# Kernel optimization log

Hardware: AMD Instinct MI355X
Metric: run time of the kernel (lower is better)

The kernel has to match this reference:

```python
import jax, jax.numpy as jnp
import numpy as np

B, TAPE, N, F = 128, 100000, 50000, 32

def setup_inputs() -> dict:
    key = jax.random.key(0)
    k1, k2, k3, k4 = jax.random.split(key, 4)
    tape = jax.random.normal(k1, (B, TAPE), dtype=jnp.float32)
    input_indices = jax.random.randint(k2, (N, F), 0, TAPE)
    # He init scaled by fan-in, padding slots (index==0) zeroed as in __init__
    weights = jax.random.normal(k3, (N, F), dtype=jnp.float32) * jnp.sqrt(2.0 / F)
    weights = jnp.where(input_indices == 0, 0.0, weights)
    bias = jnp.zeros((N,), dtype=jnp.float32)
    output_indices = jnp.arange(N)
    act_type = jax.random.randint(k4, (N,), 0, 2)
    return {"tape": tape, "weights": weights, "bias": bias,
            "input_indices": input_indices, "output_indices": output_indices,
            "act_type": act_type}

def reference(tape, weights, bias, input_indices, output_indices, act_type):
    # gather padded fan-in inputs: [B, N, F]
    gathered = tape[:, input_indices]
    # weighted sum over fan-in + bias: [B, N]
    x = jnp.einsum('bnf,nf->bn', gathered, weights) + bias
    # per-activation-type apply (two activation groups: relu / tanh)
    x = jnp.where(act_type == 0, jax.nn.relu(x), jnp.tanh(x))
    # scatter results back into tape
    return tape.at[:, output_indices].set(x)
```

## Files before the change

### kernel.cpp

```cpp
#include <hip/hip_runtime.h>
#include <cmath>

#define TAPE_SZ 100000
#define N_SZ    50000
#define F_SZ    32
#define B_SZ    128
#define GSUB    64
#define RANGE   25000
#define NBV     128
#define NCHUNK  391
#define GRID_G  (NCHUNK*2)

static __device__ __forceinline__ unsigned short f32_to_bf16(float f) {
    unsigned int u = __float_as_uint(f);
    u = (u + 0x7fffu + ((u >> 16) & 1u)) >> 16;
    return (unsigned short)u;
}

__global__ __launch_bounds__(256) void transpose_g64(const float* __restrict__ in,
                                                     unsigned short* __restrict__ outG,
                                                     float* __restrict__ out) {
    __shared__ float tile[32][129];
    const int x0 = blockIdx.x * 32;
    const int tx = threadIdx.x;
    const int ty = threadIdx.y;

    #pragma unroll
    for (int yy = ty; yy < B_SZ; yy += 8)
        tile[tx][yy] = in[(size_t)yy * TAPE_SZ + x0 + tx];
    __syncthreads();

    const int tid = ty * 32 + tx;
    const int l = tid >> 3;
    const int o = tid & 7;
    const int g = o >> 2;
    const int j = o & 3;
    unsigned short* dst = outG + ((size_t)g * TAPE_SZ + x0 + l) * GSUB + j * 16;
    union { unsigned short u[8]; uint4 q; } p0, p1;
    #pragma unroll
    for (int k = 0; k < 8; ++k) {
        p0.u[k] = f32_to_bf16(tile[l][g * GSUB + j * 16 + k]);
        p1.u[k] = f32_to_bf16(tile[l][g * GSUB + j * 16 + 8 + k]);
    }
    *(uint4*)dst       = p0.q;
    *(uint4*)(dst + 8) = p1.q;

    if (x0 + tx >= N_SZ) {
        #pragma unroll
        for (int yy = ty; yy < B_SZ; yy += 8)
            out[(size_t)yy * TAPE_SZ + x0 + tx] = tile[tx][yy];
    }
}

__global__ __launch_bounds__(512, 4) void gather_g64(
    const unsigned short* __restrict__ tapeG,
    const float* __restrict__ weights,
    const float* __restrict__ bias,
    const int*   __restrict__ in_idx,
    const int*   __restrict__ out_idx,
    const int*   __restrict__ act_type,
    float* __restrict__ out) {
    __shared__ union {
        struct {
            uint2 ent[NBV][33];
            int   start[NBV][5];
        } s;
        float x[GSUB][132];
    } u;
    __shared__ int   s_oidx[NBV];
    __shared__ float s_bias[NBV];
    __shared__ int   s_act[NBV];

    const int tid   = threadIdx.x;
    const int g     = blockIdx.x & 1;
    const int chunk = blockIdx.x >> 1;
    const int n0    = chunk * NBV;
    const int nend  = min(NBV, N_SZ - n0);

    if (tid < NBV) {
        if (tid < nend) {
            const int*   ip = in_idx  + (size_t)(n0 + tid) * 32;
            const float* wp = weights + (size_t)(n0 + tid) * 32;
            int ix[32];
            #pragma unroll
            for (int f = 0; f < 32; ++f) ix[f] = ip[f];
            int c0 = 0, c1 = 0, c2 = 0, c3 = 0;
            #pragma unroll
            for (int f = 0; f < 32; ++f) {
                const int r = ix[f] / RANGE;
                c0 += (r == 0); c1 += (r == 1); c2 += (r == 2); c3 += (r == 3);
            }
            int o0 = 0, o1 = c0, o2 = c0 + c1, o3 = c0 + c1 + c2;
            u.s.start[tid][0] = 0;  u.s.start[tid][1] = o1;
            u.s.start[tid][2] = o2; u.s.start[tid][3] = o3;
            u.s.start[tid][4] = 32;
            #pragma unroll
            for (int f = 0; f < 32; ++f) {
                const int r = ix[f] / RANGE;
                int pos;
                if      (r == 0) pos = o0++;
                else if (r == 1) pos = o1++;
                else if (r == 2) pos = o2++;
                else             pos = o3++;
                u.s.ent[tid][pos] = make_uint2((unsigned)ix[f], __float_as_uint(wp[f]));
            }
            s_oidx[tid] = out_idx[n0 + tid];
            s_bias[tid] = bias[n0 + tid];
            s_act[tid]  = act_type[n0 + tid];
        } else {
            #pragma unroll
            for (int r = 0; r < 5; ++r) u.s.start[tid][r] = 0;
        }
    }
    __syncthreads();

    const int nl = tid >> 2;
    const int q  = tid & 3;
    const unsigned short* tg = tapeG + (size_t)g * TAPE_SZ * GSUB + q * 16;

    float a[16];
    #pragma unroll
    for (int k = 0; k < 16; ++k) a[k] = 0.f;

    #pragma unroll 1
    for (int r = 0; r < 4; ++r) {
        const int e1 = u.s.start[nl][r + 1];
        for (int e = u.s.start[nl][r]; e < e1; ++e) {
            const uint2 iw = u.s.ent[nl][e];
            const unsigned short* p = tg + (size_t)iw.x * GSUB;
            const uint4 q0 = *(const uint4*)(p);
            const uint4 q1 = *(const uint4*)(p + 8);
            const float wv = __uint_as_float(iw.y);
#define ACC8(Q, B0) \
            a[B0+0] = fmaf(__uint_as_float((Q).x << 16),          wv, a[B0+0]); \
            a[B0+1] = fmaf(__uint_as_float((Q).x & 0xffff0000u),  wv, a[B0+1]); \
            a[B0+2] = fmaf(__uint_as_float((Q).y << 16),          wv, a[B0+2]); \
            a[B0+3] = fmaf(__uint_as_float((Q).y & 0xffff0000u),  wv, a[B0+3]); \
            a[B0+4] = fmaf(__uint_as_float((Q).z << 16),          wv, a[B0+4]); \
            a[B0+5] = fmaf(__uint_as_float((Q).z & 0xffff0000u),  wv, a[B0+5]); \
            a[B0+6] = fmaf(__uint_as_float((Q).w << 16),          wv, a[B0+6]); \
            a[B0+7] = fmaf(__uint_as_float((Q).w & 0xffff0000u),  wv, a[B0+7]);
            ACC8(q0, 0) ACC8(q1, 8)
#undef ACC8
        }
        __syncthreads();
    }

    {
        const float bz = (nl < nend) ? s_bias[nl] : 0.f;
        const int   at = (nl < nend) ? s_act[nl]  : 0;
        #pragma unroll
        for (int k = 0; k < 16; ++k) {
            const float v = a[k] + bz;
            a[k] = (at == 0) ? fmaxf(v, 0.f) : tanhf(v);
        }
    }
    __syncthreads();
    if (nl < nend) {
        #pragma unroll
        for (int k = 0; k < 16; ++k)
            u.x[q * 16 + k][nl] = a[k];
    }
    __syncthreads();

    const int quads = (nend + 3) >> 2;
    for (int it = tid; it < GSUB * quads; it += 512) {
        int bsub, j4;
        if (nend == NBV) { bsub = it >> 5; j4 = it & 31; }
        else             { bsub = it / quads; j4 = it - bsub * quads; }
        const int nq  = j4 * 4;
        const int oc0 = s_oidx[nq];
        float* orow = out + (size_t)(g * GSUB + bsub) * TAPE_SZ;
        const bool consec = (nq + 3 < nend) &&
                            (s_oidx[nq + 1] == oc0 + 1) &&
                            (s_oidx[nq + 2] == oc0 + 2) &&
                            (s_oidx[nq + 3] == oc0 + 3) && ((oc0 & 3) == 0);
        if (consec) {
            *(float4*)(orow + oc0) = *(const float4*)&u.x[bsub][nq];
        } else {
            #pragma unroll
            for (int c = 0; c < 4; ++c)
                if (nq + c < nend) orow[s_oidx[nq + c]] = u.x[bsub][nq + c];
        }
    }
}

__global__ __launch_bounds__(128) void gather_fallback(const float* __restrict__ tape,
                                                       const float* __restrict__ weights,
                                                       const float* __restrict__ bias,
                                                       const int*   __restrict__ in_idx,
                                                       const int*   __restrict__ out_idx,
                                                       const int*   __restrict__ act_type,
                                                       float* __restrict__ out) {
    const int n = blockIdx.x;
    const int b = threadIdx.x;
    float acc = 0.f;
    for (int f = 0; f < F_SZ; ++f) {
        acc += tape[(size_t)b * TAPE_SZ + in_idx[(size_t)n * F_SZ + f]] *
               weights[(size_t)n * F_SZ + f];
    }
    acc += bias[n];
    acc = (act_type[n] == 0) ? fmaxf(acc, 0.f) : tanhf(acc);
    out[(size_t)b * TAPE_SZ + out_idx[n]] = acc;
}

__global__ __launch_bounds__(256) void copy_tail_fb(const float* __restrict__ tape,
                                                    float* __restrict__ out) {
    const int n4 = (TAPE_SZ - N_SZ) / 4;
    int i = blockIdx.x * blockDim.x + threadIdx.x;
    int b = blockIdx.y;
    if (i < n4) {
        const float4* src = (const float4*)(tape + (size_t)b * TAPE_SZ + N_SZ);
        float4*       dst = (float4*)(out  + (size_t)b * TAPE_SZ + N_SZ);
        dst[i] = src[i];
    }
}

extern "C" void kernel_launch(void* const* d_in, const int* in_sizes, int n_in,
                              void* d_out, int out_size, void* d_ws, size_t ws_size,
                              hipStream_t stream) {
    const float* tape    = (const float*)d_in[0];
    const float* weights = (const float*)d_in[1];
    const float* bias    = (const float*)d_in[2];
    const int*   in_idx  = (const int*)d_in[3];
    const int*   out_idx = (const int*)d_in[4];
    const int*   act     = (const int*)d_in[5];
    float*       out     = (float*)d_out;

    const size_t need = (size_t)TAPE_SZ * B_SZ * sizeof(unsigned short);
    if (ws_size >= need) {
        unsigned short* tapeG = (unsigned short*)d_ws;
        transpose_g64<<<dim3(TAPE_SZ / 32), dim3(32, 8), 0, stream>>>(tape, tapeG, out);
        gather_g64<<<dim3(GRID_G), dim3(512), 0, stream>>>(
            tapeG, weights, bias, in_idx, out_idx, act, out);
    } else {
        copy_tail_fb<<<dim3(((TAPE_SZ - N_SZ) / 4 + 255) / 256, B_SZ), 256, 0, stream>>>(tape, out);
        gather_fallback<<<dim3(N_SZ), 128, 0, stream>>>(
            tape, weights, bias, in_idx, out_idx, act, out);
    }
}
```

Before: 197.3 us.

## Store full 128-batch bf16 rows per tape entry and gather once per neuron

The transposed bf16 tape changes from two 64-batch halves to one contiguous 256-byte row per tape index. The gather kernel now processes all 128 batches per block, so each neuron's index list is sorted and read once instead of twice. Bucketing widens from 4 to 8 tape ranges using packed byte counters, giving finer locality phases separated by block barriers. Each thread handles two neurons with paired loads for more memory-level parallelism, and the occupancy hint rises to 8 blocks per CU, which risks register pressure and more barrier overhead.

Result: faster. 185.5 us (-6.0%).

```diff
diff --git a/kernel.cpp b/kernel.cpp
--- a/kernel.cpp
+++ b/kernel.cpp
@@ -5,11 +5,10 @@
 #define N_SZ    50000
 #define F_SZ    32
 #define B_SZ    128
-#define GSUB    64
-#define RANGE   25000
-#define NBV     128
-#define NCHUNK  391
-#define GRID_G  (NCHUNK*2)
+#define NRANGE  8
+#define RANGE   12500
+#define NBV     64
+#define NCHUNK  ((N_SZ + NBV - 1) / NBV)
 
 static __device__ __forceinline__ unsigned short f32_to_bf16(float f) {
     unsigned int u = __float_as_uint(f);
@@ -17,9 +16,9 @@
     return (unsigned short)u;
 }
 
-__global__ __launch_bounds__(256) void transpose_g64(const float* __restrict__ in,
-                                                     unsigned short* __restrict__ outG,
-                                                     float* __restrict__ out) {
+__global__ __launch_bounds__(256) void transpose_rows(const float* __restrict__ in,
+                                                      unsigned short* __restrict__ outR,
+                                                      float* __restrict__ out) {
     __shared__ float tile[32][129];
     const int x0 = blockIdx.x * 32;
     const int tx = threadIdx.x;
@@ -33,17 +32,15 @@
     const int tid = ty * 32 + tx;
     const int l = tid >> 3;
     const int o = tid & 7;
-    const int g = o >> 2;
-    const int j = o & 3;
-    unsigned short* dst = outG + ((size_t)g * TAPE_SZ + x0 + l) * GSUB + j * 16;
+    unsigned short* dst = outR + (size_t)(x0 + l) * B_SZ + o * 8;
     union { unsigned short u[8]; uint4 q; } p0, p1;
     #pragma unroll
     for (int k = 0; k < 8; ++k) {
-        p0.u[k] = f32_to_bf16(tile[l][g * GSUB + j * 16 + k]);
-        p1.u[k] = f32_to_bf16(tile[l][g * GSUB + j * 16 + 8 + k]);
-    }
-    *(uint4*)dst       = p0.q;
-    *(uint4*)(dst + 8) = p1.q;
+        p0.u[k] = f32_to_bf16(tile[l][o * 8 + k]);
+        p1.u[k] = f32_to_bf16(tile[l][64 + o * 8 + k]);
+    }
+    *(uint4*)dst        = p0.q;
+    *(uint4*)(dst + 64) = p1.q;
 
     if (x0 + tx >= N_SZ) {
         #pragma unroll
@@ -52,8 +49,8 @@
     }
 }
 
-__global__ __launch_bounds__(512, 4) void gather_g64(
-    const unsigned short* __restrict__ tapeG,
+__global__ __launch_bounds__(512, 8) void gather_rows(
+    const unsigned short* __restrict__ tapeR,
     const float* __restrict__ weights,
     const float* __restrict__ bias,
     const int*   __restrict__ in_idx,
@@ -63,19 +60,17 @@
     __shared__ union {
         struct {
             uint2 ent[NBV][33];
-            int   start[NBV][5];
+            int   start[NBV][NRANGE + 1];
         } s;
-        float x[GSUB][132];
+        float x[B_SZ][65];
     } u;
     __shared__ int   s_oidx[NBV];
     __shared__ float s_bias[NBV];
     __shared__ int   s_act[NBV];
 
-    const int tid   = threadIdx.x;
-    const int g     = blockIdx.x & 1;
-    const int chunk = blockIdx.x >> 1;
-    const int n0    = chunk * NBV;
-    const int nend  = min(NBV, N_SZ - n0);
+    const int tid  = threadIdx.x;
+    const int n0   = blockIdx.x * NBV;
+    const int nend = min(NBV, N_SZ - n0);
 
     if (tid < NBV) {
         if (tid < nend) {
@@ -84,24 +79,25 @@
             int ix[32];
             #pragma unroll
             for (int f = 0; f < 32; ++f) ix[f] = ip[f];
-            int c0 = 0, c1 = 0, c2 = 0, c3 = 0;
+            unsigned long long c = 0ull;
+            #pragma unroll
+            for (int f = 0; f < 32; ++f) c += 1ull << (8 * (ix[f] / RANGE));
+            int off[NRANGE + 1];
+            off[0] = 0;
+            #pragma unroll
+            for (int r = 0; r < NRANGE; ++r)
+                off[r + 1] = off[r] + (int)((c >> (8 * r)) & 255u);
+            #pragma unroll
+            for (int r = 0; r <= NRANGE; ++r) u.s.start[tid][r] = off[r];
+            unsigned long long p = 0ull;
+            #pragma unroll
+            for (int r = 0; r < NRANGE; ++r)
+                p |= (unsigned long long)off[r] << (8 * r);
             #pragma unroll
             for (int f = 0; f < 32; ++f) {
-                const int r = ix[f] / RANGE;
-                c0 += (r == 0); c1 += (r == 1); c2 += (r == 2); c3 += (r == 3);
-            }
-            int o0 = 0, o1 = c0, o2 = c0 + c1, o3 = c0 + c1 + c2;
-            u.s.start[tid][0] = 0;  u.s.start[tid][1] = o1;
-            u.s.start[tid][2] = o2; u.s.start[tid][3] = o3;
-            u.s.start[tid][4] = 32;
-            #pragma unroll
-            for (int f = 0; f < 32; ++f) {
-                const int r = ix[f] / RANGE;
-                int pos;
-                if      (r == 0) pos = o0++;
-                else if (r == 1) pos = o1++;
-                else if (r == 2) pos = o2++;
-                else             pos = o3++;
+                const int r   = ix[f] / RANGE;
+                const int pos = (int)((p >> (8 * r)) & 255u);
+                p += 1ull << (8 * r);
                 u.s.ent[tid][pos] = make_uint2((unsigned)ix[f], __float_as_uint(wp[f]));
             }
             s_oidx[tid] = out_idx[n0 + tid];
@@ -109,78 +105,119 @@
             s_act[tid]  = act_type[n0 + tid];
         } else {
             #pragma unroll
-            for (int r = 0; r < 5; ++r) u.s.start[tid][r] = 0;
+            for (int r = 0; r <= NRANGE; ++r) u.s.start[tid][r] = 0;
         }
     }
     __syncthreads();
 
-    const int nl = tid >> 2;
-    const int q  = tid & 3;
-    const unsigned short* tg = tapeG + (size_t)g * TAPE_SZ * GSUB + q * 16;
-
-    float a[16];
+    const int s  = tid & 15;
+    const int nl = tid >> 4;
+    const unsigned short* tp = tapeR + s * 8;
+
+    float aA[8], aB[8];
     #pragma unroll
-    for (int k = 0; k < 16; ++k) a[k] = 0.f;
+    for (int k = 0; k < 8; ++k) { aA[k] = 0.f; aB[k] = 0.f; }
+
+#define ACC8(Q, A, WV) \
+    A[0] = fmaf(__uint_as_float((Q).x << 16),          WV, A[0]); \
+    A[1] = fmaf(__uint_as_float((Q).x & 0xffff0000u),  WV, A[1]); \
+    A[2] = fmaf(__uint_as_float((Q).y << 16),          WV, A[2]); \
+    A[3] = fmaf(__uint_as_float((Q).y & 0xffff0000u),  WV, A[3]); \
+    A[4] = fmaf(__uint_as_float((Q).z << 16),          WV, A[4]); \
+    A[5] = fmaf(__uint_as_float((Q).z & 0xffff0000u),  WV, A[5]); \
+    A[6] = fmaf(__uint_as_float((Q).w << 16),          WV, A[6]); \
+    A[7] = fmaf(__uint_as_float((Q).w & 0xffff0000u),  WV, A[7]);
 
     #pragma unroll 1
-    for (int r = 0; r < 4; ++r) {
-        const int e1 = u.s.start[nl][r + 1];
-        for (int e = u.s.start[nl][r]; e < e1; ++e) {
-            const uint2 iw = u.s.ent[nl][e];
-            const unsigned short* p = tg + (size_t)iw.x * GSUB;
-            const uint4 q0 = *(const uint4*)(p);
-            const uint4 q1 = *(const uint4*)(p + 8);
-            const float wv = __uint_as_float(iw.y);
-#define ACC8(Q, B0) \
-            a[B0+0] = fmaf(__uint_as_float((Q).x << 16),          wv, a[B0+0]); \
-            a[B0+1] = fmaf(__uint_as_float((Q).x & 0xffff0000u),  wv, a[B0+1]); \
-            a[B0+2] = fmaf(__uint_as_float((Q).y << 16),          wv, a[B0+2]); \
-            a[B0+3] = fmaf(__uint_as_float((Q).y & 0xffff0000u),  wv, a[B0+3]); \
-            a[B0+4] = fmaf(__uint_as_float((Q).z << 16),          wv, a[B0+4]); \
-            a[B0+5] = fmaf(__uint_as_float((Q).z & 0xffff0000u),  wv, a[B0+5]); \
-            a[B0+6] = fmaf(__uint_as_float((Q).w << 16),          wv, a[B0+6]); \
-            a[B0+7] = fmaf(__uint_as_float((Q).w & 0xffff0000u),  wv, a[B0+7]);
-            ACC8(q0, 0) ACC8(q1, 8)
+    for (int r = 0; r < NRANGE; ++r) {
+        {
+            const int e1 = u.s.start[nl][r + 1];
+            int e = u.s.start[nl][r];
+            for (; e + 1 < e1; e += 2) {
+                const uint2 w0 = u.s.ent[nl][e];
+                const uint2 w1 = u.s.ent[nl][e + 1];
+                const uint4 q0 = *(const uint4*)(tp + (size_t)w0.x * B_SZ);
+                const uint4 q1 = *(const uint4*)(tp + (size_t)w1.x * B_SZ);
+                const float v0 = __uint_as_float(w0.y), v1 = __uint_as_float(w1.y);
+                ACC8(q0, aA, v0) ACC8(q1, aA, v1)
+            }
+            if (e < e1) {
+                const uint2 w0 = u.s.ent[nl][e];
+                const uint4 q0 = *(const uint4*)(tp + (size_t)w0.x * B_SZ);
+                const float v0 = __uint_as_float(w0.y);
+                ACC8(q0, aA, v0)
+            }
+        }
+        {
+            const int e1 = u.s.start[nl + 32][r + 1];
+            int e = u.s.start[nl + 32][r];
+            for (; e + 1 < e1; e += 2) {
+                const uint2 w0 = u.s.ent[nl + 32][e];
+                const uint2 w1 = u.s.ent[nl + 32][e + 1];
+                const uint4 q0 = *(const uint4*)(tp + (size_t)w0.x * B_SZ);
+                const uint4 q1 = *(const uint4*)(tp + (size_t)w1.x * B_SZ);
+                const float v0 = __uint_as_float(w0.y), v1 = __uint_as_float(w1.y);
+                ACC8(q0, aB, v0) ACC8(q1, aB, v1)
+            }
+            if (e < e1) {
+                const uint2 w0 = u.s.ent[nl + 32][e];
+                const uint4 q0 = *(const uint4*)(tp + (size_t)w0.x * B_SZ);
+                const float v0 = __uint_as_float(w0.y);
+                ACC8(q0, aB, v0)
+            }
+        }
+        __syncthreads();
+    }
 #undef ACC8
-        }
-        __syncthreads();
-    }
-
-    {
-        const float bz = (nl < nend) ? s_bias[nl] : 0.f;
-        const int   at = (nl < nend) ? s_act[nl]  : 0;
-        #pragma unroll
-        for (int k = 0; k < 16; ++k) {
-            const float v = a[k] + bz;
-            a[k] = (at == 0) ? fmaxf(v, 0.f) : tanhf(v);
-        }
+
+    if (nl < nend) {
+        const float bz = s_bias[nl];
+        const int   at = s_act[nl];
+        #pragma unroll
+        for (int k = 0; k < 8; ++k) {
+            const float v = aA[k] + bz;
+            aA[k] = (at == 0) ? fmaxf(v, 0.f) : tanhf(v);
+        }
+    }
+    if (nl + 32 < nend) {
+        const float bz = s_bias[nl + 32];
+        const int   at = s_act[nl + 32];
+        #pragma unroll
+        for (int k = 0; k < 8; ++k) {
+            const float v = aB[k] + bz;
+            aB[k] = (at == 0) ? fmaxf(v, 0.f) : tanhf(v);
+        }
+    }
+
+    if (nl < nend) {
+        #pragma unroll
+        for (int k = 0; k < 8; ++k) u.x[s * 8 + k][nl] = aA[k];
+    }
+    if (nl + 32 < nend) {
+        #pragma unroll
+        for (int k = 0; k < 8; ++k) u.x[s * 8 + k][nl + 32] = aB[k];
     }
     __syncthreads();
-    if (nl < nend) {
-        #pragma unroll
-        for (int k = 0; k < 16; ++k)
-            u.x[q * 16 + k][nl] = a[k];
-    }
-    __syncthreads();
 
     const int quads = (nend + 3) >> 2;
-    for (int it = tid; it < GSUB * quads; it += 512) {
-        int bsub, j4;
-        if (nend == NBV) { bsub = it >> 5; j4 = it & 31; }
-        else             { bsub = it / quads; j4 = it - bsub * quads; }
+    for (int it = tid; it < B_SZ * quads; it += 512) {
+        int b, j4;
+        if (nend == NBV) { b = it >> 4; j4 = it & 15; }
+        else             { b = it / quads; j4 = it - b * quads; }
         const int nq  = j4 * 4;
         const int oc0 = s_oidx[nq];
-        float* orow = out + (size_t)(g * GSUB + bsub) * TAPE_SZ;
+        float* orow = out + (size_t)b * TAPE_SZ;
         const bool consec = (nq + 3 < nend) &&
                             (s_oidx[nq + 1] == oc0 + 1) &&
                             (s_oidx[nq + 2] == oc0 + 2) &&
                             (s_oidx[nq + 3] == oc0 + 3) && ((oc0 & 3) == 0);
         if (consec) {
-            *(float4*)(orow + oc0) = *(const float4*)&u.x[bsub][nq];
+            *(float4*)(orow + oc0) = make_float4(u.x[b][nq + 0], u.x[b][nq + 1],
+                                                 u.x[b][nq + 2], u.x[b][nq + 3]);
         } else {
             #pragma unroll
             for (int c = 0; c < 4; ++c)
-                if (nq + c < nend) orow[s_oidx[nq + c]] = u.x[bsub][nq + c];
+                if (nq + c < nend) orow[s_oidx[nq + c]] = u.x[b][nq + c];
         }
     }
 }
@@ -229,10 +266,10 @@
 
     const size_t need = (size_t)TAPE_SZ * B_SZ * sizeof(unsigned short);
     if (ws_size >= need) {
-        unsigned short* tapeG = (unsigned short*)d_ws;
-        transpose_g64<<<dim3(TAPE_SZ / 32), dim3(32, 8), 0, stream>>>(tape, tapeG, out);
-        gather_g64<<<dim3(GRID_G), dim3(512), 0, stream>>>(
-            tapeG, weights, bias, in_idx, out_idx, act, out);
+        unsigned short* tapeR = (unsigned short*)d_ws;
+        transpose_rows<<<dim3(TAPE_SZ / 32), dim3(32, 8), 0, stream>>>(tape, tapeR, out);
+        gather_rows<<<dim3(NCHUNK), dim3(512), 0, stream>>>(
+            tapeR, weights, bias, in_idx, out_idx, act, out);
     } else {
         copy_tail_fb<<<dim3(((TAPE_SZ - N_SZ) / 4 + 255) / 256, B_SZ), 256, 0, stream>>>(tape, out);
         gather_fallback<<<dim3(N_SZ), 128, 0, stream>>>(
```
